# Optimization experiments

Measured on AMD Instinct MI355X. Metric: run time of the kernel, lower is better.

The kernel has to match this reference:

```python
import jax, jax.numpy as jnp
import numpy as np

N = 50000      # nodes
E = 800000     # edges (before self-loops)
H = 4          # attention heads
C = 64         # hidden_dim per head
F_IN = 8       # node_features
NEG_SLOPE = 0.2  # PyG GATConv default


def setup_inputs() -> dict:
    key = jax.random.key(0)
    ks = jax.random.split(key, 16)
    def g(k, shape, fan_in):
        return (jax.random.normal(k, shape, jnp.float32) / np.sqrt(fan_in)).astype(jnp.float32)
    x = jax.random.normal(ks[0], (N, F_IN), jnp.float32)
    edge_index = jax.random.randint(ks[1], (2, E), 0, N, dtype=jnp.int32)
    # GATConv params: layer 0 maps F_IN->H*C, layers 1,2 map H*C->H*C
    W0 = g(ks[2], (F_IN, H * C), F_IN)
    Ws = g(ks[3], (2, H * C, H * C), H * C)
    att_src = g(ks[4], (3, H, C), C)
    att_dst = g(ks[5], (3, H, C), C)
    bconv = jnp.zeros((3, H * C), jnp.float32)
    # order / time predictor MLPs: Linear(256,64) -> ReLU -> Linear(64,1)
    ow1 = g(ks[6], (H * C, C), H * C); ob1 = jnp.zeros((C,), jnp.float32)
    ow2 = g(ks[7], (C, 1), C);         ob2 = jnp.zeros((1,), jnp.float32)
    tw1 = g(ks[8], (H * C, C), H * C); tb1 = jnp.zeros((C,), jnp.float32)
    tw2 = g(ks[9], (C, 1), C);         tb2 = jnp.zeros((1,), jnp.float32)
    return {"x": x, "edge_index": edge_index, "W0": W0, "Ws": Ws,
            "att_src": att_src, "att_dst": att_dst, "bconv": bconv,
            "ow1": ow1, "ob1": ob1, "ow2": ow2, "ob2": ob2,
            "tw1": tw1, "tb1": tb1, "tw2": tw2, "tb2": tb2}


def _gat_layer(h_in, src, dst, W, a_src, a_dst, b):
    """PyG-style GATConv (concat heads, eval mode, self-loops already in src/dst)."""
    h = (h_in @ W).reshape(N, H, C)                       # [N,H,C]
    al_s = jnp.einsum('nhc,hc->nh', h, a_src)             # [N,H]
    al_d = jnp.einsum('nhc,hc->nh', h, a_dst)             # [N,H]
    e = jax.nn.leaky_relu(al_s[src] + al_d[dst], NEG_SLOPE)  # [Etot,H]
    m = jax.ops.segment_max(e, dst, num_segments=N)       # segment-softmax over in-edges
    ee = jnp.exp(e - m[dst])
    den = jax.ops.segment_sum(ee, dst, num_segments=N)
    alpha = ee / den[dst]                                 # [Etot,H]
    out = jax.ops.segment_sum(h[src] * alpha[:, :, None], dst, num_segments=N)
    return out.reshape(N, H * C) + b


def reference(x, edge_index, W0, Ws, att_src, att_dst, bconv,
              ow1, ob1, ow2, ob2, tw1, tb1, tw2, tb2):
    loops = jnp.arange(N, dtype=edge_index.dtype)
    src = jnp.concatenate([edge_index[0], loops])
    dst = jnp.concatenate([edge_index[1], loops])
    h = _gat_layer(x, src, dst, W0, att_src[0], att_dst[0], bconv[0])
    h = jax.nn.relu(h)   # dropout is identity in eval
    h = _gat_layer(h, src, dst, Ws[0], att_src[1], att_dst[1], bconv[1])
    h = jax.nn.relu(h)
    h = _gat_layer(h, src, dst, Ws[1], att_src[2], att_dst[2], bconv[2])
    order_scores = jax.nn.relu(h @ ow1 + ob1) @ ow2 + ob2  # [N,1]
    time_scores = jax.nn.relu(h @ tw1 + tb1) @ tw2 + tb2   # [N,1]
    return (order_scores, time_scores)
```

## Files before the change

kernel.cpp:

```cpp
#include <hip/hip_runtime.h>
#include <hip/hip_bf16.h>
#include <hip/hip_fp16.h>

#define NN 50000
#define EE 800000
#define ET 850000
#define HH 4
#define CC 64
#define HC 256
#define DMAX 64

using f16v8 = __attribute__((ext_vector_type(8))) _Float16;
using f32v4 = __attribute__((ext_vector_type(4))) float;

__device__ __forceinline__ float4 cvt_h4(uint2 raw) {
    __half2 a = *reinterpret_cast<__half2*>(&raw.x);
    __half2 b = *reinterpret_cast<__half2*>(&raw.y);
    float2 fa = __half22float2(a), fb = __half22float2(b);
    return make_float4(fa.x, fa.y, fb.x, fb.y);
}

__global__ void k_bucket(const int* __restrict__ ei, int* __restrict__ cnt,
                         unsigned short* __restrict__ esrc) {
    int e = blockIdx.x * blockDim.x + threadIdx.x;
    if (e < ET) {
        int d, s;
        if (e < EE) { d = ei[EE + e]; s = ei[e]; }
        else        { d = e - EE;     s = d; }
        int pos = atomicAdd(&cnt[d], 1);
        if (pos < DMAX)
            __builtin_nontemporal_store((unsigned short)s,
                                        &esrc[(size_t)d * DMAX + pos]);
    }
}

#define G0B  3125
#define G0_NODES 16
__global__ __launch_bounds__(256) void k_prep_gemm0(
        const float* __restrict__ Ws, const float* __restrict__ ow1,
        const float* __restrict__ tw1, __half* __restrict__ Wt,
        __half* __restrict__ Wh,
        const float* __restrict__ x, const float* __restrict__ W0,
        const float* __restrict__ asrc, const float* __restrict__ adst,
        __half* __restrict__ hg, float* __restrict__ al_s,
        float* __restrict__ al_d) {
    __shared__ float sx[G0_NODES * 8];
    int b = blockIdx.x;
    if (b < G0B) {
        int t = threadIdx.x;
        int n0 = b * G0_NODES;
        float w[8];
#pragma unroll
        for (int k = 0; k < 8; k++) w[k] = W0[k * HC + t];
        float as = asrc[t], ad = adst[t];
        int lane = t & 63, wv = t >> 6;
        if (t < G0_NODES * 8) sx[t] = x[(size_t)n0 * 8 + t];
        __syncthreads();
        for (int ni = 0; ni < G0_NODES; ni++) {
            int n = n0 + ni;
            float acc = 0.f;
#pragma unroll
            for (int k = 0; k < 8; k++) acc += sx[ni * 8 + k] * w[k];
            hg[(size_t)n * HC + t] = __float2half(acc);
            float s = acc * as, d = acc * ad;
            for (int off = 32; off > 0; off >>= 1) {
                s += __shfl_down(s, off, 64);
                d += __shfl_down(d, off, 64);
            }
            if (lane == 0) { al_s[n * HH + wv] = s; al_d[n * HH + wv] = d; }
        }
        return;
    }
    b -= G0B;
    int i = b * 256 + threadIdx.x;
    if (i < 2 * HC * HC) {
        int m = i >> 16;
        int n = (i >> 8) & 255;
        int k = i & 255;
        Wt[i] = __float2half(Ws[m * HC * HC + k * HC + n]);
    }
    int j = i - 2 * HC * HC;
    if (j >= 0 && j < 128 * HC) {
        int c = j >> 8;
        int k = j & 255;
        float v = (c < 64) ? ow1[k * CC + c] : tw1[k * CC + (c - 64)];
        Wh[j] = __float2half(v);
    }
}

#define GM 128
#define GN 128
#define GK 64
__global__ __launch_bounds__(256) void k_gemmh(const __half* __restrict__ A,
                                               const __half* __restrict__ Bt,
                                               const float* __restrict__ asrc,
                                               const float* __restrict__ adst,
                                               __half* __restrict__ hg,
                                               float* __restrict__ al_s,
                                               float* __restrict__ al_d) {
    __shared__ __half As[GM][GK + 8];
    __shared__ __half Bs[GN][GK + 8];
    int t = threadIdx.x;
    int l = t & 63, wv = t >> 6;
    int wm = wv >> 1, wn = wv & 1;
    int row0 = blockIdx.x * GM;
    int col0 = blockIdx.y * GN;
    f32v4 acc[4][4] = {};
    const __half* Ab = A + (size_t)row0 * HC;
    const __half* Bb = Bt + (size_t)col0 * HC;
    int sr = t >> 3, sc = (t & 7) * 8;
    for (int k0 = 0; k0 < HC; k0 += GK) {
#pragma unroll
        for (int i = 0; i < 4; i++) {
            int rr = sr + i * 32;
            uint4 v = {0u, 0u, 0u, 0u};
            if (row0 + rr < NN) v = *(const uint4*)(Ab + (size_t)rr * HC + k0 + sc);
            *(uint4*)&As[rr][sc] = v;
            *(uint4*)&Bs[rr][sc] = *(const uint4*)(Bb + (size_t)rr * HC + k0 + sc);
        }
        __syncthreads();
#pragma unroll
        for (int kk = 0; kk < GK; kk += 32) {
            f16v8 af[4], bf[4];
#pragma unroll
            for (int i = 0; i < 4; i++)
                af[i] = *(const f16v8*)&As[wm * 64 + i * 16 + (l & 15)][kk + (l >> 4) * 8];
#pragma unroll
            for (int j = 0; j < 4; j++)
                bf[j] = *(const f16v8*)&Bs[wn * 64 + j * 16 + (l & 15)][kk + (l >> 4) * 8];
#pragma unroll
            for (int i = 0; i < 4; i++)
#pragma unroll
                for (int j = 0; j < 4; j++)
                    acc[i][j] = __builtin_amdgcn_mfma_f32_16x16x32_f16(af[i], bf[j], acc[i][j], 0, 0, 0);
        }
        __syncthreads();
    }
    int head = (col0 >> 6) + wn;
    float va[4], vd[4];
#pragma unroll
    for (int j = 0; j < 4; j++) {
        int c = j * 16 + (l & 15);
        va[j] = asrc[head * CC + c];
        vd[j] = adst[head * CC + c];
    }
    int cbase = col0 + wn * 64 + (l & 15);
#pragma unroll
    for (int i = 0; i < 4; i++) {
#pragma unroll
        for (int v = 0; v < 4; v++) {
            int r = row0 + wm * 64 + i * 16 + (l >> 4) * 4 + v;
            bool ok = (r < NN);
            float s = 0.f, d = 0.f;
#pragma unroll
            for (int j = 0; j < 4; j++) {
                float xv = acc[i][j][v];
                s += xv * va[j];
                d += xv * vd[j];
                if (ok) hg[(size_t)r * HC + cbase + j * 16] = __float2half(xv);
            }
            s += __shfl_xor(s, 8, 16); d += __shfl_xor(d, 8, 16);
            s += __shfl_xor(s, 4, 16); d += __shfl_xor(d, 4, 16);
            s += __shfl_xor(s, 2, 16); d += __shfl_xor(d, 2, 16);
            s += __shfl_xor(s, 1, 16); d += __shfl_xor(d, 1, 16);
            if (ok && (l & 15) == 0) {
                al_s[r * HH + head] = s;
                al_d[r * HH + head] = d;
            }
        }
    }
}

__global__ __launch_bounds__(256) void k_fagg(const int* __restrict__ cnt,
                                              const unsigned short* __restrict__ esrc,
                                              const float* __restrict__ al_s,
                                              const float* __restrict__ al_d,
                                              const __half* __restrict__ hg,
                                              const float* __restrict__ bias,
                                              __half* __restrict__ out, int do_relu) {
    __shared__ float s_p[4][HH][72];
    __shared__ int   s_src[4][64];
    int t = threadIdx.x;
    int wv = t >> 6, l = t & 63;
    int n = blockIdx.x * 4 + wv;
    int myh = l >> 4;
    int beg = n * DMAX;
    int end = beg + cnt[n];
    float4 ad = *(const float4*)&al_d[(size_t)n * HH];
    float den = 0.f;
    float4 acc = {0.f, 0.f, 0.f, 0.f};
    const __half* hgl = hg + l * 4;

    for (int off = beg; off < end; off += 64) {
        int csize = min(64, end - off);
        float4 pp = {0.f, 0.f, 0.f, 0.f};
        int s = 0;
        if (l < csize) {
            s = (int)esrc[(size_t)off + l];
            float4 as = *(const float4*)&al_s[(size_t)s * HH];
            float v;
            v = as.x + ad.x; pp.x = __expf((v > 0.f) ? v : 0.2f * v);
            v = as.y + ad.y; pp.y = __expf((v > 0.f) ? v : 0.2f * v);
            v = as.z + ad.z; pp.z = __expf((v > 0.f) ? v : 0.2f * v);
            v = as.w + ad.w; pp.w = __expf((v > 0.f) ? v : 0.2f * v);
        }
        s_src[wv][l] = s;
        s_p[wv][0][l] = pp.x;
        s_p[wv][1][l] = pp.y;
        s_p[wv][2][l] = pp.z;
        s_p[wv][3][l] = pp.w;
        const float* prow = s_p[wv][myh];
        const int*   srow = s_src[wv];
        int k = 0;
        for (; k + 8 <= csize; k += 8) {
            int si[8];
#pragma unroll
            for (int u = 0; u < 8; u++) si[u] = srow[k + u];
            uint2 rw[8];
#pragma unroll
            for (int u = 0; u < 8; u++) rw[u] = *(const uint2*)&hgl[(size_t)si[u] * HC];
            float p[8];
#pragma unroll
            for (int u = 0; u < 8; u++) p[u] = prow[k + u];
#pragma unroll
            for (int u = 0; u < 8; u++) {
                float4 v = cvt_h4(rw[u]);
                den += p[u];
                acc.x += p[u] * v.x;
                acc.y += p[u] * v.y;
                acc.z += p[u] * v.z;
                acc.w += p[u] * v.w;
            }
        }
        for (; k + 4 <= csize; k += 4) {
            int si[4];
#pragma unroll
            for (int u = 0; u < 4; u++) si[u] = srow[k + u];
            uint2 rw[4];
#pragma unroll
            for (int u = 0; u < 4; u++) rw[u] = *(const uint2*)&hgl[(size_t)si[u] * HC];
            float p[4];
#pragma unroll
            for (int u = 0; u < 4; u++) p[u] = prow[k + u];
#pragma unroll
            for (int u = 0; u < 4; u++) {
                float4 v = cvt_h4(rw[u]);
                den += p[u];
                acc.x += p[u] * v.x;
                acc.y += p[u] * v.y;
                acc.z += p[u] * v.z;
                acc.w += p[u] * v.w;
            }
        }
        for (; k < csize; k++) {
            float p = prow[k];
            float4 v = cvt_h4(*(const uint2*)&hgl[(size_t)srow[k] * HC]);
            den += p;
            acc.x += p * v.x; acc.y += p * v.y; acc.z += p * v.z; acc.w += p * v.w;
        }
    }

    float4 b = *(const float4*)&bias[l * 4];
    float inv = 1.f / den;
    float4 o;
    o.x = acc.x * inv + b.x; o.y = acc.y * inv + b.y;
    o.z = acc.z * inv + b.z; o.w = acc.w * inv + b.w;
    if (do_relu) {
        o.x = fmaxf(o.x, 0.f); o.y = fmaxf(o.y, 0.f);
        o.z = fmaxf(o.z, 0.f); o.w = fmaxf(o.w, 0.f);
    }
    union { __half h[4]; uint2 u; } pk;
    pk.h[0] = __float2half(o.x); pk.h[1] = __float2half(o.y);
    pk.h[2] = __float2half(o.z); pk.h[3] = __float2half(o.w);
    *(uint2*)&out[(size_t)n * HC + l * 4] = pk.u;
}

__global__ __launch_bounds__(256) void k_headh(const __half* __restrict__ A,
                                               const __half* __restrict__ Wh,
                                               const float* __restrict__ ob1,
                                               const float* __restrict__ ow2,
                                               const float* __restrict__ ob2,
                                               const float* __restrict__ tb1,
                                               const float* __restrict__ tw2,
                                               const float* __restrict__ tb2,
                                               float* __restrict__ out) {
    __shared__ __half As[GM][GK + 8];
    __shared__ __half Bs[GN][GK + 8];
    int t = threadIdx.x;
    int l = t & 63, wv = t >> 6;
    int wm = wv >> 1, wn = wv & 1;
    int row0 = blockIdx.x * GM;
    f32v4 acc[4][4] = {};
    const __half* Ab = A + (size_t)row0 * HC;
    int sr = t >> 3, sc = (t & 7) * 8;
    for (int k0 = 0; k0 < HC; k0 += GK) {
#pragma unroll
        for (int i = 0; i < 4; i++) {
            int rr = sr + i * 32;
            uint4 v = {0u, 0u, 0u, 0u};
            if (row0 + rr < NN) v = *(const uint4*)(Ab + (size_t)rr * HC + k0 + sc);
            *(uint4*)&As[rr][sc] = v;
            *(uint4*)&Bs[rr][sc] = *(const uint4*)(Wh + (size_t)rr * HC + k0 + sc);
        }
        __syncthreads();
#pragma unroll
        for (int kk = 0; kk < GK; kk += 32) {
            f16v8 af[4], bf[4];
#pragma unroll
            for (int i = 0; i < 4; i++)
                af[i] = *(const f16v8*)&As[wm * 64 + i * 16 + (l & 15)][kk + (l >> 4) * 8];
#pragma unroll
            for (int j = 0; j < 4; j++)
                bf[j] = *(const f16v8*)&Bs[wn * 64 + j * 16 + (l & 15)][kk + (l >> 4) * 8];
#pragma unroll
            for (int i = 0; i < 4; i++)
#pragma unroll
                for (int j = 0; j < 4; j++)
                    acc[i][j] = __builtin_amdgcn_mfma_f32_16x16x32_f16(af[i], bf[j], acc[i][j], 0, 0, 0);
        }
        __syncthreads();
    }
    float b1[4], w2[4];
#pragma unroll
    for (int j = 0; j < 4; j++) {
        int c = j * 16 + (l & 15);
        b1[j] = wn ? tb1[c] : ob1[c];
        w2[j] = wn ? tw2[c] : ow2[c];
    }
    float b2 = wn ? tb2[0] : ob2[0];
#pragma unroll
    for (int i = 0; i < 4; i++) {
#pragma unroll
        for (int v = 0; v < 4; v++) {
            int r = row0 + wm * 64 + i * 16 + (l >> 4) * 4 + v;
            float s = 0.f;
#pragma unroll
            for (int j = 0; j < 4; j++)
                s += fmaxf(acc[i][j][v] + b1[j], 0.f) * w2[j];
            s += __shfl_xor(s, 8, 16);
            s += __shfl_xor(s, 4, 16);
            s += __shfl_xor(s, 2, 16);
            s += __shfl_xor(s, 1, 16);
            if ((l & 15) == 0 && r < NN)
                out[(size_t)(wn ? NN : 0) + r] = s + b2;
        }
    }
}

extern "C" void kernel_launch(void* const* d_in, const int* in_sizes, int n_in,
                              void* d_out, int out_size, void* d_ws, size_t ws_size,
                              hipStream_t stream) {
    const float* x      = (const float*)d_in[0];
    const int*   ei     = (const int*)d_in[1];
    const float* W0     = (const float*)d_in[2];
    const float* Ws     = (const float*)d_in[3];
    const float* attsrc = (const float*)d_in[4];
    const float* attdst = (const float*)d_in[5];
    const float* bconv  = (const float*)d_in[6];
    const float* ow1 = (const float*)d_in[7];
    const float* ob1 = (const float*)d_in[8];
    const float* ow2 = (const float*)d_in[9];
    const float* ob2 = (const float*)d_in[10];
    const float* tw1 = (const float*)d_in[11];
    const float* tb1 = (const float*)d_in[12];
    const float* tw2 = (const float*)d_in[13];
    const float* tb2 = (const float*)d_in[14];
    float* outp = (float*)d_out;

    char* ws = (char*)d_ws;
    size_t off = 0;
    auto alloc = [&](size_t bytes) -> void* {
        void* p = ws + off;
        off += (bytes + 255) & ~(size_t)255;
        return p;
    };
    __half*         hA   = (__half*)alloc(sizeof(__half) * NN * HC);
    __half*         hB16 = (__half*)alloc(sizeof(__half) * NN * HC);
    float*          al_s = (float*)alloc(sizeof(float) * NN * HH);
    float*          al_d = (float*)alloc(sizeof(float) * NN * HH);
    int*            cnt  = (int*)alloc(sizeof(int) * NN);
    unsigned short* esrc = (unsigned short*)alloc(sizeof(unsigned short) * (size_t)NN * DMAX);
    __half*         Wt   = (__half*)alloc(sizeof(__half) * 2 * HC * HC);
    __half*         Wh   = (__half*)alloc(sizeof(__half) * 128 * HC);
    (void)ws_size; (void)in_sizes; (void)n_in; (void)out_size;

    hipMemsetAsync(cnt, 0, sizeof(int) * NN, stream);
    k_bucket<<<(ET + 255) / 256, 256, 0, stream>>>(ei, cnt, esrc);
    k_prep_gemm0<<<G0B + 640, 256, 0, stream>>>(Ws, ow1, tw1, Wt, Wh,
                                                x, W0, attsrc, attdst,
                                                hA, al_s, al_d);

    for (int l = 0; l < 3; l++) {
        if (l > 0) {
            dim3 grid((NN + GM - 1) / GM, 2);
            k_gemmh<<<grid, 256, 0, stream>>>(hB16, Wt + (size_t)(l - 1) * HC * HC,
                                              attsrc + l * HC, attdst + l * HC,
                                              hA, al_s, al_d);
        }
        k_fagg<<<NN / 4, 256, 0, stream>>>(cnt, esrc, al_s, al_d, hA,
                                           bconv + l * HC, hB16, (l < 2) ? 1 : 0);
    }

    k_headh<<<(NN + GM - 1) / GM, 256, 0, stream>>>(hB16, Wh, ob1, ow2, ob2,
                                                    tb1, tw2, tb2, outp);
}
```

Measured before the change: 363.6 us.

## Replace global-atomic edge bucketing with two-pass LDS radix binning

The single edge-bucketing kernel, which did one global atomic per edge and scattered 2-byte stores, is replaced by two passes. The first pass bins edges into coarse 256-node buckets through shared memory and flushes them in chunks to a global coarse array. The second pass builds each node's adjacency rows in LDS, inserts the self-loop first, and writes whole rows with wide stores. The aim is to cut global atomic contention and uncoalesced writes. In exchange it adds an extra kernel launch and fixed capacity limits (CCAP per bucket) that can silently drop edges, and the order of edges within a row changes.

```diff
diff --git a/kernel.cpp b/kernel.cpp
--- a/kernel.cpp
+++ b/kernel.cpp
@@ -20,18 +20,81 @@
     return make_float4(fa.x, fa.y, fb.x, fb.y);
 }
 
-__global__ void k_bucket(const int* __restrict__ ei, int* __restrict__ cnt,
-                         unsigned short* __restrict__ esrc) {
-    int e = blockIdx.x * blockDim.x + threadIdx.x;
-    if (e < ET) {
-        int d, s;
-        if (e < EE) { d = ei[EE + e]; s = ei[e]; }
-        else        { d = e - EE;     s = d; }
-        int pos = atomicAdd(&cnt[d], 1);
-        if (pos < DMAX)
-            __builtin_nontemporal_store((unsigned short)s,
-                                        &esrc[(size_t)d * DMAX + pos]);
-    }
+#define NCB 196
+#define E_PER_B 4096
+#define NB1 196
+#define BCAP 48
+#define CCAP 4608
+
+__global__ __launch_bounds__(256) void k_pass1(const int* __restrict__ ei,
+                                               int* __restrict__ ccnt,
+                                               unsigned int* __restrict__ coarse) {
+    __shared__ unsigned int lbin[NCB * BCAP];
+    __shared__ int lcnt[NCB];
+    int t = threadIdx.x, wv = t >> 6, lane = t & 63;
+    for (int i = t; i < NCB; i += 256) lcnt[i] = 0;
+    __syncthreads();
+    int e0 = blockIdx.x * E_PER_B;
+    for (int i = 0; i < E_PER_B; i += 256) {
+        int e = e0 + i + t;
+        if (e < EE) {
+            int src = ei[e];
+            int dst = ei[EE + e];
+            int bb = dst >> 8;
+            unsigned int pk = ((unsigned int)(dst & 255) << 16) | (unsigned int)src;
+            int pos = atomicAdd(&lcnt[bb], 1);
+            if (pos < BCAP) {
+                lbin[bb * BCAP + pos] = pk;
+            } else {
+                int g = atomicAdd(&ccnt[bb], 1);
+                if (g < CCAP) coarse[(size_t)bb * CCAP + g] = pk;
+            }
+        }
+    }
+    __syncthreads();
+    for (int bb = wv; bb < NCB; bb += 4) {
+        int n = min(lcnt[bb], BCAP);
+        int base = 0;
+        if (lane == 0) base = atomicAdd(&ccnt[bb], n);
+        base = __shfl(base, 0, 64);
+        if (lane < n) {
+            int g = base + lane;
+            if (g < CCAP) coarse[(size_t)bb * CCAP + g] = lbin[bb * BCAP + lane];
+        }
+    }
+}
+
+__global__ __launch_bounds__(256) void k_pass2(const int* __restrict__ ccnt,
+                                               const unsigned int* __restrict__ coarse,
+                                               int* __restrict__ cnt,
+                                               unsigned short* __restrict__ esrc) {
+    __shared__ unsigned short lrow[256 * DMAX];
+    __shared__ int lcnt2[256];
+    int b = blockIdx.x, t = threadIdx.x;
+    int node0 = b * 256;
+    if (node0 + t < NN) {
+        lrow[t * DMAX] = (unsigned short)(node0 + t);
+        lcnt2[t] = 1;
+    } else {
+        lcnt2[t] = 1;
+    }
+    __syncthreads();
+    int m = min(ccnt[b], CCAP);
+    for (int i = t; i < m; i += 256) {
+        unsigned int pk = coarse[(size_t)b * CCAP + i];
+        int dl = (pk >> 16) & 255;
+        int src = pk & 0xFFFF;
+        int pos = atomicAdd(&lcnt2[dl], 1);
+        if (pos < DMAX) lrow[dl * DMAX + pos] = (unsigned short)src;
+    }
+    __syncthreads();
+    const uint4* lr4 = (const uint4*)lrow;
+    for (int u = t; u < 2048; u += 256) {
+        int row = u >> 3;
+        if (node0 + row < NN)
+            *(uint4*)&esrc[(size_t)(node0 + row) * DMAX + (u & 7) * 8] = lr4[u];
+    }
+    if (node0 + t < NN) cnt[node0 + t] = min(lcnt2[t], DMAX);
 }
 
 #define G0B  3125
@@ -374,18 +437,21 @@
         off += (bytes + 255) & ~(size_t)255;
         return p;
     };
-    __half*         hA   = (__half*)alloc(sizeof(__half) * NN * HC);
-    __half*         hB16 = (__half*)alloc(sizeof(__half) * NN * HC);
-    float*          al_s = (float*)alloc(sizeof(float) * NN * HH);
-    float*          al_d = (float*)alloc(sizeof(float) * NN * HH);
-    int*            cnt  = (int*)alloc(sizeof(int) * NN);
-    unsigned short* esrc = (unsigned short*)alloc(sizeof(unsigned short) * (size_t)NN * DMAX);
-    __half*         Wt   = (__half*)alloc(sizeof(__half) * 2 * HC * HC);
-    __half*         Wh   = (__half*)alloc(sizeof(__half) * 128 * HC);
+    __half*         hA     = (__half*)alloc(sizeof(__half) * NN * HC);
+    __half*         hB16   = (__half*)alloc(sizeof(__half) * NN * HC);
+    float*          al_s   = (float*)alloc(sizeof(float) * NN * HH);
+    float*          al_d   = (float*)alloc(sizeof(float) * NN * HH);
+    int*            cnt    = (int*)alloc(sizeof(int) * NN);
+    unsigned short* esrc   = (unsigned short*)alloc(sizeof(unsigned short) * (size_t)NN * DMAX);
+    int*            ccnt   = (int*)alloc(sizeof(int) * NCB);
+    unsigned int*   coarse = (unsigned int*)alloc(sizeof(unsigned int) * (size_t)NCB * CCAP);
+    __half*         Wt     = (__half*)alloc(sizeof(__half) * 2 * HC * HC);
+    __half*         Wh     = (__half*)alloc(sizeof(__half) * 128 * HC);
     (void)ws_size; (void)in_sizes; (void)n_in; (void)out_size;
 
-    hipMemsetAsync(cnt, 0, sizeof(int) * NN, stream);
-    k_bucket<<<(ET + 255) / 256, 256, 0, stream>>>(ei, cnt, esrc);
+    hipMemsetAsync(ccnt, 0, sizeof(int) * NCB, stream);
+    k_pass1<<<NB1, 256, 0, stream>>>(ei, ccnt, coarse);
+    k_pass2<<<NCB, 256, 0, stream>>>(ccnt, coarse, cnt, esrc);
     k_prep_gemm0<<<G0B + 640, 256, 0, stream>>>(Ws, ow1, tw1, Wt, Wh,
                                                 x, W0, attsrc, attdst,
                                                 hA, al_s, al_d);
```

Result: slower. 511.2 us (+40.6%).
